# Kernel optimization log

Measured on AMD Instinct MI355X. Metric: run time of the kernel, lower is better.

Reference implementation:

```python
import jax, jax.numpy as jnp
import numpy as np

E = 1024      # d_model
H = 16        # num heads
D = E // H    # head dim = 64
FF = 4096     # dim_feedforward
WIN = 128
EPS = 1e-5    # layer-norm eps
NEG = -1e9


def setup_inputs() -> dict:
    key = jax.random.key(0)
    ks = jax.random.split(key, 16)
    s = 0.02
    f32 = jnp.float32
    return {
        "src":       jax.random.normal(ks[0], (2, 2048, E), f32),
        "in_proj_w": jax.random.normal(ks[1], (3 * E, E), f32) * s,
        "in_proj_b": jnp.zeros((3 * E,), f32),
        "out_w":     jax.random.normal(ks[2], (E, E), f32) * s,
        "out_b":     jnp.zeros((E,), f32),
        "lin1_w":    jax.random.normal(ks[3], (FF, E), f32) * s,
        "lin1_b":    jnp.zeros((FF,), f32),
        "lin2_w":    jax.random.normal(ks[4], (E, FF), f32) * s,
        "lin2_b":    jnp.zeros((E,), f32),
        "ln1_g":     jnp.ones((E,), f32),
        "ln1_beta":  jnp.zeros((E,), f32),
        "ln2_g":     jnp.ones((E,), f32),
        "ln2_beta":  jnp.zeros((E,), f32),
    }


def _layer_norm(x, g, b):
    mu = x.mean(-1, keepdims=True)
    var = ((x - mu) ** 2).mean(-1, keepdims=True)
    return (x - mu) * jax.lax.rsqrt(var + EPS) * g + b


def reference(src, in_proj_w, in_proj_b, out_w, out_b,
              lin1_w, lin1_b, lin2_w, lin2_b,
              ln1_g, ln1_beta, ln2_g, ln2_beta):
    B, L, _ = src.shape  # batch_first=True
    x = src

    # fused QKV projection (torch Linear: y = x @ W.T + b)
    qkv = x @ in_proj_w.T + in_proj_b            # [B, L, 3E]
    q, k, v = jnp.split(qkv, 3, axis=-1)
    q = q.reshape(B, L, H, D)
    k = k.reshape(B, L, H, D)
    v = v.reshape(B, L, H, D)

    scores = jnp.einsum('blhd,bmhd->bhlm', q, k) / np.float32(np.sqrt(D))
    idx = jnp.arange(L)
    band = jnp.abs(idx[:, None] - idx[None, :]) <= WIN   # [L, L] allowed positions
    scores = jnp.where(band, scores, NEG)
    attn = jax.nn.softmax(scores, axis=-1)

    ctx = jnp.einsum('bhlm,bmhd->blhd', attn, v).reshape(B, L, E)
    attn_out = ctx @ out_w.T + out_b

    # post-norm transformer encoder layer (norm_first=False default)
    x = _layer_norm(x + attn_out, ln1_g, ln1_beta)
    ff = jax.nn.relu(x @ lin1_w.T + lin1_b) @ lin2_w.T + lin2_b
    return _layer_norm(x + ff, ln2_g, ln2_beta)
```

## Files before the change

### kernel.cpp

```cpp
#include <hip/hip_runtime.h>
#include <cstdint>
#include <cstddef>


typedef __attribute__((ext_vector_type(8))) short short8;
typedef __attribute__((ext_vector_type(4))) float f32x4;

__device__ __forceinline__ float b2f(unsigned short u) {
  union { unsigned int i; float f; } x; x.i = ((unsigned int)u) << 16; return x.f;
}
__device__ __forceinline__ unsigned short f2b(float f) {
  union { float f; unsigned int i; } x; x.f = f;
  unsigned int i = x.i;
  unsigned int r = (i + 0x7FFFu + ((i >> 16) & 1u)) >> 16;
  return (unsigned short)r;
}
__device__ __forceinline__ uint4 pack8(float4 f0, float4 f1) {
  uint4 r;
  r.x = (unsigned)f2b(f0.x) | ((unsigned)f2b(f0.y) << 16);
  r.y = (unsigned)f2b(f0.z) | ((unsigned)f2b(f0.w) << 16);
  r.z = (unsigned)f2b(f1.x) | ((unsigned)f2b(f1.y) << 16);
  r.w = (unsigned)f2b(f1.z) | ((unsigned)f2b(f1.w) << 16);
  return r;
}

__device__ __forceinline__ void gl_lds16(const unsigned short* g, unsigned short* l) {
  __builtin_amdgcn_global_load_lds(
      (const __attribute__((address_space(1))) unsigned int*)g,
      (__attribute__((address_space(3))) unsigned int*)l, 16, 0, 0);
}

__global__ __launch_bounds__(256) void conv_k(
    const float* __restrict__ in, unsigned short* __restrict__ out, int n)
{
  const int i = (blockIdx.x * 256 + threadIdx.x) * 8;
  if (i < n) {
    const float4 f0 = *(const float4*)(in + i);
    const float4 f1 = *(const float4*)(in + i + 4);
    *(uint4*)(out + i) = pack8(f0, f1);
  }
}

template<int RELU, int OUT32>
__global__ __launch_bounds__(256) void gemm128(
    const unsigned short* __restrict__ A, const unsigned short* __restrict__ Wb,
    const float* __restrict__ bias, void* __restrict__ out,
    int M, int N, int K)
{
  __shared__ unsigned short As[2][128 * 64];
  __shared__ unsigned short Bs[2][128 * 64];

  const int tid = threadIdx.x;
  const int lane = tid & 63, wid = tid >> 6;

  const int nwgx = gridDim.x;
  const int flat = blockIdx.y * nwgx + blockIdx.x;
  const int chunk = (nwgx * gridDim.y) >> 3;
  const int nf = (flat & 7) * chunk + (flat >> 3);
  const int m0 = (nf / nwgx) * 128, n0 = (nf % nwgx) * 128;

  const unsigned short* gA[4];
  const unsigned short* gW[4];
  int ldsO[4];
#pragma unroll
  for (int i = 0; i < 4; ++i) {
    const int sl = wid * 256 + i * 64 + lane;
    const int r = sl >> 3, s = sl & 7, c = (s + r) & 7;
    gA[i] = A + (size_t)(m0 + r) * K + c * 8;
    gW[i] = Wb + (size_t)(n0 + r) * K + c * 8;
    ldsO[i] = (wid * 256 + i * 64) * 8;
  }

  const int cl = lane & 15;
  const int kg = lane >> 4;
  const int msub = (wid >> 1) * 64, nsub = (wid & 1) * 64;
  int aoff[4][2], boff[4][2];
#pragma unroll
  for (int t = 0; t < 4; ++t) {
    const int ar = msub + t * 16 + cl;
    const int br = nsub + t * 16 + cl;
#pragma unroll
    for (int ks = 0; ks < 2; ++ks) {
      aoff[t][ks] = ar * 64 + ((ks * 4 + kg - ar) & 7) * 8;
      boff[t][ks] = br * 64 + ((ks * 4 + kg - br) & 7) * 8;
    }
  }

  f32x4 acc[4][4];
#pragma unroll
  for (int i = 0; i < 4; ++i)
#pragma unroll
    for (int j = 0; j < 4; ++j) acc[i][j] = (f32x4){0.f, 0.f, 0.f, 0.f};

  const int steps = K >> 6;

  const int pre = steps < 2 ? steps : 2;
  for (int t = 0; t < pre; ++t) {
#pragma unroll
    for (int i = 0; i < 4; ++i) { gl_lds16(gA[i], &As[t][ldsO[i]]); gA[i] += 64; }
#pragma unroll
    for (int i = 0; i < 4; ++i) { gl_lds16(gW[i], &Bs[t][ldsO[i]]); gW[i] += 64; }
  }

  int cur = 0;
  for (int s = 0; s < steps; ++s) {
    if (s + 1 < steps) asm volatile("s_waitcnt vmcnt(8)" ::: "memory");
    else               asm volatile("s_waitcnt vmcnt(0)" ::: "memory");
    __builtin_amdgcn_s_barrier();

    short8 af[4][2], bf[4][2];
#pragma unroll
    for (int t = 0; t < 4; ++t) {
      af[t][0] = *(const short8*)&As[cur][aoff[t][0]];
      bf[t][0] = *(const short8*)&Bs[cur][boff[t][0]];
    }
#pragma unroll
    for (int t = 0; t < 4; ++t) {
      af[t][1] = *(const short8*)&As[cur][aoff[t][1]];
      bf[t][1] = *(const short8*)&Bs[cur][boff[t][1]];
    }

    __builtin_amdgcn_s_setprio(1);
#pragma unroll
    for (int mt = 0; mt < 4; ++mt)
#pragma unroll
      for (int nt = 0; nt < 4; ++nt)
        acc[mt][nt] = __builtin_amdgcn_mfma_f32_16x16x32_bf16(af[mt][0], bf[nt][0], acc[mt][nt], 0, 0, 0);
    __builtin_amdgcn_s_setprio(0);

    asm volatile("s_waitcnt lgkmcnt(0)" ::: "memory");
    __builtin_amdgcn_sched_barrier(0);
    __builtin_amdgcn_s_barrier();

    if (s + 2 < steps) {
#pragma unroll
      for (int i = 0; i < 4; ++i) { gl_lds16(gA[i], &As[cur][ldsO[i]]); gA[i] += 64; }
#pragma unroll
      for (int i = 0; i < 4; ++i) { gl_lds16(gW[i], &Bs[cur][ldsO[i]]); gW[i] += 64; }
    }

    __builtin_amdgcn_s_setprio(1);
#pragma unroll
    for (int mt = 0; mt < 4; ++mt)
#pragma unroll
      for (int nt = 0; nt < 4; ++nt)
        acc[mt][nt] = __builtin_amdgcn_mfma_f32_16x16x32_bf16(af[mt][1], bf[nt][1], acc[mt][nt], 0, 0, 0);
    __builtin_amdgcn_s_setprio(0);

    cur ^= 1;
  }

#pragma unroll
  for (int nt = 0; nt < 4; ++nt) {
    const int col = n0 + nsub + nt * 16 + cl;
    const float bvs = bias[col];
#pragma unroll
    for (int mt = 0; mt < 4; ++mt) {
#pragma unroll
      for (int r = 0; r < 4; ++r) {
        const int grow = m0 + msub + mt * 16 + kg * 4 + r;
        float v = acc[mt][nt][r] + bvs;
        if (RELU) v = fmaxf(v, 0.f);
        if (OUT32) ((float*)out)[(size_t)grow * N + col] = v;
        else       ((unsigned short*)out)[(size_t)grow * N + col] = f2b(v);
      }
    }
  }
}

template<int OUT32>
__global__ __launch_bounds__(256) void gemm64(
    const unsigned short* __restrict__ A, const unsigned short* __restrict__ Wb,
    const float* __restrict__ bias, void* __restrict__ out,
    int M, int N, int K)
{
  __shared__ unsigned short As[3][64 * 64];
  __shared__ unsigned short Bs[3][128 * 64];

  const int tid = threadIdx.x;
  const int lane = tid & 63, wid = tid >> 6;

  const int nwgx = gridDim.x;
  const int flat = blockIdx.y * nwgx + blockIdx.x;
  const int chunk = (nwgx * gridDim.y) >> 3;
  const int nf = (flat & 7) * chunk + (flat >> 3);
  const int m0 = (nf / nwgx) * 64, n0 = (nf % nwgx) * 128;

  const unsigned short* gA[2];
  const unsigned short* gW[4];
  int ldsA[2], ldsB[4];
#pragma unroll
  for (int i = 0; i < 2; ++i) {
    const int sl = wid * 128 + i * 64 + lane;
    const int r = sl >> 3, s = sl & 7, c = (s + r) & 7;
    gA[i] = A + (size_t)(m0 + r) * K + c * 8;
    ldsA[i] = (wid * 128 + i * 64) * 8;
  }
#pragma unroll
  for (int i = 0; i < 4; ++i) {
    const int sl = wid * 256 + i * 64 + lane;
    const int r = sl >> 3, s = sl & 7, c = (s + r) & 7;
    gW[i] = Wb + (size_t)(n0 + r) * K + c * 8;
    ldsB[i] = (wid * 256 + i * 64) * 8;
  }

  const int cl = lane & 15;
  const int kg = lane >> 4;
  int aoff[4][2], boff[2][2];
#pragma unroll
  for (int t = 0; t < 4; ++t) {
    const int ar = t * 16 + cl;
#pragma unroll
    for (int ks = 0; ks < 2; ++ks)
      aoff[t][ks] = ar * 64 + ((ks * 4 + kg - ar) & 7) * 8;
  }
#pragma unroll
  for (int t = 0; t < 2; ++t) {
    const int br = wid * 32 + t * 16 + cl;
#pragma unroll
    for (int ks = 0; ks < 2; ++ks)
      boff[t][ks] = br * 64 + ((ks * 4 + kg - br) & 7) * 8;
  }

  f32x4 acc[4][2];
#pragma unroll
  for (int i = 0; i < 4; ++i)
#pragma unroll
    for (int j = 0; j < 2; ++j) acc[i][j] = (f32x4){0.f, 0.f, 0.f, 0.f};

  const int steps = K >> 6;

  const int pre = steps < 3 ? steps : 3;
  for (int t = 0; t < pre; ++t) {
#pragma unroll
    for (int i = 0; i < 2; ++i) { gl_lds16(gA[i], &As[t][ldsA[i]]); gA[i] += 64; }
#pragma unroll
    for (int i = 0; i < 4; ++i) { gl_lds16(gW[i], &Bs[t][ldsB[i]]); gW[i] += 64; }
  }

  int cur = 0;
  for (int s = 0; s < steps; ++s) {
    const int rem = steps - 1 - s;
    if (rem >= 2)      asm volatile("s_waitcnt vmcnt(12)" ::: "memory");
    else if (rem == 1) asm volatile("s_waitcnt vmcnt(6)" ::: "memory");
    else               asm volatile("s_waitcnt vmcnt(0)" ::: "memory");
    __builtin_amdgcn_s_barrier();

    short8 af[4][2], bf[2][2];
#pragma unroll
    for (int t = 0; t < 4; ++t) af[t][0] = *(const short8*)&As[cur][aoff[t][0]];
#pragma unroll
    for (int t = 0; t < 2; ++t) bf[t][0] = *(const short8*)&Bs[cur][boff[t][0]];
#pragma unroll
    for (int t = 0; t < 4; ++t) af[t][1] = *(const short8*)&As[cur][aoff[t][1]];
#pragma unroll
    for (int t = 0; t < 2; ++t) bf[t][1] = *(const short8*)&Bs[cur][boff[t][1]];

    __builtin_amdgcn_s_setprio(1);
#pragma unroll
    for (int mt = 0; mt < 4; ++mt)
#pragma unroll
      for (int nt = 0; nt < 2; ++nt)
        acc[mt][nt] = __builtin_amdgcn_mfma_f32_16x16x32_bf16(af[mt][0], bf[nt][0], acc[mt][nt], 0, 0, 0);
    __builtin_amdgcn_s_setprio(0);

    asm volatile("s_waitcnt lgkmcnt(0)" ::: "memory");
    __builtin_amdgcn_sched_barrier(0);
    __builtin_amdgcn_s_barrier();

    if (s + 3 < steps) {
#pragma unroll
      for (int i = 0; i < 2; ++i) { gl_lds16(gA[i], &As[cur][ldsA[i]]); gA[i] += 64; }
#pragma unroll
      for (int i = 0; i < 4; ++i) { gl_lds16(gW[i], &Bs[cur][ldsB[i]]); gW[i] += 64; }
    }

    __builtin_amdgcn_s_setprio(1);
#pragma unroll
    for (int mt = 0; mt < 4; ++mt)
#pragma unroll
      for (int nt = 0; nt < 2; ++nt)
        acc[mt][nt] = __builtin_amdgcn_mfma_f32_16x16x32_bf16(af[mt][1], bf[nt][1], acc[mt][nt], 0, 0, 0);
    __builtin_amdgcn_s_setprio(0);

    cur = (cur == 2) ? 0 : cur + 1;
  }

#pragma unroll
  for (int nt = 0; nt < 2; ++nt) {
    const int col = n0 + wid * 32 + nt * 16 + cl;
    const float bvs = bias[col];
#pragma unroll
    for (int mt = 0; mt < 4; ++mt) {
#pragma unroll
      for (int r = 0; r < 4; ++r) {
        const int grow = m0 + mt * 16 + kg * 4 + r;
        const float v = acc[mt][nt][r] + bvs;
        if (OUT32) ((float*)out)[(size_t)grow * N + col] = v;
        else       ((unsigned short*)out)[(size_t)grow * N + col] = f2b(v);
      }
    }
  }
}

__global__ __launch_bounds__(256) void attn_mfma(
    const unsigned short* __restrict__ qkv, unsigned short* __restrict__ ctx)
{
  __shared__ unsigned short Ks[64 * 72];
  __shared__ unsigned short Vt[64 * 72];
  __shared__ unsigned short Ps[64 * 72];

  const int tid = threadIdx.x;
  const int bid = blockIdx.x;
  const int qt = bid & 31, h = (bid >> 5) & 15, b = bid >> 9;
  const int q0 = qt * 64;
  const int wstart = max(0, q0 - 128);
  const int wend = min(2048, q0 + 64 + 128);
  const int ntile = (wend - wstart + 63) >> 6;
  const size_t rowb = (size_t)b * 2048;

  const int lane = tid & 63, wid = tid >> 6;
  const int cl = lane & 15;
  const int kq = (lane >> 4) * 8;
  const int rowg = lane >> 4;

  short8 aQ[2];
#pragma unroll
  for (int ks = 0; ks < 2; ++ks)
    aQ[ks] = *(const short8*)(qkv + (rowb + q0 + wid * 16 + cl) * 3072 + h * 64 + ks * 32 + kq);

  float m_i[4], l_i[4];
  f32x4 O[4];
#pragma unroll
  for (int r = 0; r < 4; ++r) { m_i[r] = -1.0e30f; l_i[r] = 0.f; }
#pragma unroll
  for (int nt = 0; nt < 4; ++nt) O[nt] = (f32x4){0.f, 0.f, 0.f, 0.f};

  for (int t = 0; t < ntile; ++t) {
    const int jbase = wstart + t * 64;
    __syncthreads();
    for (int idx = tid; idx < 512; idx += 256) {
      const int r = idx >> 3, c = idx & 7;
      const int jg = jbase + r;
      uint4 kv = {0u, 0u, 0u, 0u}, vv = {0u, 0u, 0u, 0u};
      if (jg < wend) {
        const size_t base = (rowb + jg) * 3072 + h * 64 + c * 8;
        kv = *(const uint4*)(qkv + base + 1024);
        vv = *(const uint4*)(qkv + base + 2048);
      }
      *(uint4*)&Ks[r * 72 + c * 8] = kv;
      const unsigned short* vs = (const unsigned short*)&vv;
#pragma unroll
      for (int ii = 0; ii < 8; ++ii) Vt[(c * 8 + ii) * 72 + r] = vs[ii];
    }
    __syncthreads();

    f32x4 S[4];
#pragma unroll
    for (int nt = 0; nt < 4; ++nt) S[nt] = (f32x4){0.f, 0.f, 0.f, 0.f};
#pragma unroll
    for (int nt = 0; nt < 4; ++nt)
#pragma unroll
      for (int ks = 0; ks < 2; ++ks) {
        const short8 bK = *(const short8*)&Ks[(nt * 16 + cl) * 72 + ks * 32 + kq];
        S[nt] = __builtin_amdgcn_mfma_f32_16x16x32_bf16(aQ[ks], bK, S[nt], 0, 0, 0);
      }

    float sc[4][4];
#pragma unroll
    for (int nt = 0; nt < 4; ++nt) {
      const int jg = jbase + nt * 16 + cl;
#pragma unroll
      for (int r = 0; r < 4; ++r) {
        const int i = q0 + wid * 16 + rowg * 4 + r;
        const bool v = (jg < wend) && (jg >= i - 128) && (jg <= i + 128);
        sc[nt][r] = v ? S[nt][r] * 0.125f : -1.0e30f;
      }
    }

    float alpha[4], p[4][4];
#pragma unroll
    for (int r = 0; r < 4; ++r) {
      float tm = fmaxf(fmaxf(sc[0][r], sc[1][r]), fmaxf(sc[2][r], sc[3][r]));
      tm = fmaxf(tm, __shfl_xor(tm, 1, 64));
      tm = fmaxf(tm, __shfl_xor(tm, 2, 64));
      tm = fmaxf(tm, __shfl_xor(tm, 4, 64));
      tm = fmaxf(tm, __shfl_xor(tm, 8, 64));
      const float mn = fmaxf(m_i[r], tm);
      alpha[r] = __expf(m_i[r] - mn);
      m_i[r] = mn;
      float ps = 0.f;
#pragma unroll
      for (int nt = 0; nt < 4; ++nt) { p[nt][r] = __expf(sc[nt][r] - mn); ps += p[nt][r]; }
      ps += __shfl_xor(ps, 1, 64);
      ps += __shfl_xor(ps, 2, 64);
      ps += __shfl_xor(ps, 4, 64);
      ps += __shfl_xor(ps, 8, 64);
      l_i[r] = l_i[r] * alpha[r] + ps;
    }

#pragma unroll
    for (int nt = 0; nt < 4; ++nt)
#pragma unroll
      for (int r = 0; r < 4; ++r)
        Ps[(wid * 16 + rowg * 4 + r) * 72 + nt * 16 + cl] = f2b(p[nt][r]);
    __syncthreads();

#pragma unroll
    for (int nt = 0; nt < 4; ++nt)
#pragma unroll
      for (int r = 0; r < 4; ++r) O[nt][r] *= alpha[r];
    short8 aP[2];
#pragma unroll
    for (int ks = 0; ks < 2; ++ks)
      aP[ks] = *(const short8*)&Ps[(wid * 16 + cl) * 72 + ks * 32 + kq];
#pragma unroll
    for (int nt = 0; nt < 4; ++nt)
#pragma unroll
      for (int ks = 0; ks < 2; ++ks) {
        const short8 bV = *(const short8*)&Vt[(nt * 16 + cl) * 72 + ks * 32 + kq];
        O[nt] = __builtin_amdgcn_mfma_f32_16x16x32_bf16(aP[ks], bV, O[nt], 0, 0, 0);
      }
  }

#pragma unroll
  for (int nt = 0; nt < 4; ++nt) {
    const int d = nt * 16 + cl;
#pragma unroll
    for (int r = 0; r < 4; ++r) {
      const int i = q0 + wid * 16 + rowg * 4 + r;
      ctx[(rowb + i) * 1024 + h * 64 + d] = f2b(O[nt][r] / l_i[r]);
    }
  }
}

template<int AF32, int BF32, int OF32>
__global__ __launch_bounds__(256) void ln_k(
    const void* __restrict__ a, const void* __restrict__ b,
    const float* __restrict__ g, const float* __restrict__ be,
    void* __restrict__ o)
{
  __shared__ float rbuf[8];
  const int tid = threadIdx.x;
  const size_t base = (size_t)blockIdx.x * 1024;
  const int lane = tid & 63, wid = tid >> 6;

  float xv[4], s = 0.f, sq = 0.f;
#pragma unroll
  for (int t = 0; t < 4; ++t) {
    const int c = tid + t * 256;
    const float av = AF32 ? ((const float*)a)[base + c]
                          : b2f(((const unsigned short*)a)[base + c]);
    const float bv = BF32 ? ((const float*)b)[base + c]
                          : b2f(((const unsigned short*)b)[base + c]);
    const float x = av + bv;
    xv[t] = x; s += x; sq += x * x;
  }
  for (int o2 = 1; o2 < 64; o2 <<= 1) { s += __shfl_xor(s, o2, 64); sq += __shfl_xor(sq, o2, 64); }
  if (lane == 0) { rbuf[wid] = s; rbuf[wid + 4] = sq; }
  __syncthreads();
  s  = rbuf[0] + rbuf[1] + rbuf[2] + rbuf[3];
  sq = rbuf[4] + rbuf[5] + rbuf[6] + rbuf[7];
  const float mean = s * (1.0f / 1024.f);
  const float var = sq * (1.0f / 1024.f) - mean * mean;
  const float rstd = rsqrtf(var + 1e-5f);
#pragma unroll
  for (int t = 0; t < 4; ++t) {
    const int c = tid + t * 256;
    const float y = (xv[t] - mean) * rstd * g[c] + be[c];
    if (OF32) ((float*)o)[base + c] = y;
    else      ((unsigned short*)o)[base + c] = f2b(y);
  }
}

extern "C" void kernel_launch(void* const* d_in, const int* in_sizes, int n_in,
                              void* d_out, int out_size, void* d_ws, size_t ws_size,
                              hipStream_t stream)
{
  (void)in_sizes; (void)n_in; (void)out_size; (void)ws_size;
  const float* src   = (const float*)d_in[0];
  const float* w_in  = (const float*)d_in[1];
  const float* b_in  = (const float*)d_in[2];
  const float* w_out = (const float*)d_in[3];
  const float* b_out = (const float*)d_in[4];
  const float* w1    = (const float*)d_in[5];
  const float* b1    = (const float*)d_in[6];
  const float* w2    = (const float*)d_in[7];
  const float* b2    = (const float*)d_in[8];
  const float* g1    = (const float*)d_in[9];
  const float* be1   = (const float*)d_in[10];
  const float* g2    = (const float*)d_in[11];
  const float* be2   = (const float*)d_in[12];

  char* ws = (char*)d_ws;
  unsigned short* srcb  = (unsigned short*)(ws);
  unsigned short* x1b   = srcb;
  unsigned short* qkv   = (unsigned short*)(ws + 8388608);
  unsigned short* ctx   = (unsigned short*)(ws + 33554432);
  unsigned short* attnb = (unsigned short*)(ws + 8388608);
  unsigned short* ff1   = (unsigned short*)(ws + 8388608);
  unsigned short* wslot = (unsigned short*)(ws + 41943040);
  float*          outf  = (float*)d_out;

  conv_k<<<dim3(2048), 256, 0, stream>>>(src, srcb, 4194304);
  conv_k<<<dim3(1536), 256, 0, stream>>>(w_in, wslot, 3145728);
  gemm128<0, 0><<<dim3(24, 32), 256, 0, stream>>>(srcb, wslot, b_in, qkv, 4096, 3072, 1024);
  attn_mfma<<<dim3(1024), 256, 0, stream>>>(qkv, ctx);
  conv_k<<<dim3(512), 256, 0, stream>>>(w_out, wslot, 1048576);
  gemm64<0><<<dim3(8, 64), 256, 0, stream>>>(ctx, wslot, b_out, attnb, 4096, 1024, 1024);
  ln_k<0, 0, 0><<<dim3(4096), 256, 0, stream>>>(srcb, attnb, g1, be1, x1b);
  conv_k<<<dim3(2048), 256, 0, stream>>>(w1, wslot, 4194304);
  gemm128<1, 0><<<dim3(32, 32), 256, 0, stream>>>(x1b, wslot, b1, ff1, 4096, 4096, 1024);
  conv_k<<<dim3(2048), 256, 0, stream>>>(w2, wslot, 4194304);
  gemm64<1><<<dim3(8, 64), 256, 0, stream>>>(ff1, wslot, b2, outf, 4096, 1024, 4096);
  ln_k<0, 1, 1><<<dim3(4096), 256, 0, stream>>>(x1b, outf, g2, be2, outf);
}
```

Before: 315.3 us.

## Enlarge QKV/FF1 GEMM tiles to 256x256 with 8 waves; reschedule gemm64 MFMAs

Replaces the 128x128, 256-thread GEMM with a 256x256-tile, 512-thread kernel. Each of its 2x4 waves computes a 128x64 sub-tile in two halves, and the fragment loads for the second half are interleaved with the first half's MFMAs. The goal is more data reuse per global byte loaded. In gemm64, all fragments are now loaded before the barrier and all MFMAs issue after the next prefetch, with the setprio hints removed. The trade-off: the large tile needs 128KB of LDS, and the QKV launch drops to 192 workgroups, which underfills the CU count and risks poor occupancy.

```diff
diff --git a/kernel.cpp b/kernel.cpp
--- a/kernel.cpp
+++ b/kernel.cpp
@@ -42,53 +42,43 @@
 }
 
 template<int RELU, int OUT32>
-__global__ __launch_bounds__(256) void gemm128(
+__global__ __launch_bounds__(512, 2) void gemm256(
     const unsigned short* __restrict__ A, const unsigned short* __restrict__ Wb,
     const float* __restrict__ bias, void* __restrict__ out,
     int M, int N, int K)
 {
-  __shared__ unsigned short As[2][128 * 64];
-  __shared__ unsigned short Bs[2][128 * 64];
+  __shared__ unsigned short As[2][256 * 64];
+  __shared__ unsigned short Bs[2][256 * 64];
 
   const int tid = threadIdx.x;
   const int lane = tid & 63, wid = tid >> 6;
-
-  const int nwgx = gridDim.x;
-  const int flat = blockIdx.y * nwgx + blockIdx.x;
-  const int chunk = (nwgx * gridDim.y) >> 3;
+  const int wm = wid >> 2, wn = wid & 3;
+
+  const int gx = gridDim.x;
+  const int flat = blockIdx.y * gx + blockIdx.x;
+  const int chunk = (gx * gridDim.y) >> 3;
   const int nf = (flat & 7) * chunk + (flat >> 3);
-  const int m0 = (nf / nwgx) * 128, n0 = (nf % nwgx) * 128;
+  const int m0 = (nf / gx) * 256, n0 = (nf % gx) * 256;
 
   const unsigned short* gA[4];
   const unsigned short* gW[4];
   int ldsO[4];
 #pragma unroll
   for (int i = 0; i < 4; ++i) {
-    const int sl = wid * 256 + i * 64 + lane;
+    const int sbase = i * 512 + (tid & ~63);
+    const int sl = sbase + lane;
     const int r = sl >> 3, s = sl & 7, c = (s + r) & 7;
     gA[i] = A + (size_t)(m0 + r) * K + c * 8;
     gW[i] = Wb + (size_t)(n0 + r) * K + c * 8;
-    ldsO[i] = (wid * 256 + i * 64) * 8;
+    ldsO[i] = sbase * 8;
   }
 
   const int cl = lane & 15;
   const int kg = lane >> 4;
-  const int msub = (wid >> 1) * 64, nsub = (wid & 1) * 64;
-  int aoff[4][2], boff[4][2];
-#pragma unroll
-  for (int t = 0; t < 4; ++t) {
-    const int ar = msub + t * 16 + cl;
-    const int br = nsub + t * 16 + cl;
-#pragma unroll
-    for (int ks = 0; ks < 2; ++ks) {
-      aoff[t][ks] = ar * 64 + ((ks * 4 + kg - ar) & 7) * 8;
-      boff[t][ks] = br * 64 + ((ks * 4 + kg - br) & 7) * 8;
-    }
-  }
-
-  f32x4 acc[4][4];
-#pragma unroll
-  for (int i = 0; i < 4; ++i)
+
+  f32x4 acc[8][4];
+#pragma unroll
+  for (int i = 0; i < 8; ++i)
 #pragma unroll
     for (int j = 0; j < 4; ++j) acc[i][j] = (f32x4){0.f, 0.f, 0.f, 0.f};
 
@@ -108,25 +98,41 @@
     else               asm volatile("s_waitcnt vmcnt(0)" ::: "memory");
     __builtin_amdgcn_s_barrier();
 
-    short8 af[4][2], bf[4][2];
-#pragma unroll
-    for (int t = 0; t < 4; ++t) {
-      af[t][0] = *(const short8*)&As[cur][aoff[t][0]];
-      bf[t][0] = *(const short8*)&Bs[cur][boff[t][0]];
-    }
-#pragma unroll
-    for (int t = 0; t < 4; ++t) {
-      af[t][1] = *(const short8*)&As[cur][aoff[t][1]];
-      bf[t][1] = *(const short8*)&Bs[cur][boff[t][1]];
-    }
+    short8 bf[4][2];
+#pragma unroll
+    for (int nt = 0; nt < 4; ++nt)
+#pragma unroll
+      for (int ks = 0; ks < 2; ++ks) {
+        const int br = wn * 64 + nt * 16 + cl;
+        bf[nt][ks] = *(const short8*)&Bs[cur][br * 64 + (((ks * 4 + kg) - br) & 7) * 8];
+      }
+    short8 af[4][2];
+#pragma unroll
+    for (int mt = 0; mt < 4; ++mt)
+#pragma unroll
+      for (int ks = 0; ks < 2; ++ks) {
+        const int ar = wm * 128 + mt * 16 + cl;
+        af[mt][ks] = *(const short8*)&As[cur][ar * 64 + (((ks * 4 + kg) - ar) & 7) * 8];
+      }
 
     __builtin_amdgcn_s_setprio(1);
 #pragma unroll
     for (int mt = 0; mt < 4; ++mt)
 #pragma unroll
       for (int nt = 0; nt < 4; ++nt)
-        acc[mt][nt] = __builtin_amdgcn_mfma_f32_16x16x32_bf16(af[mt][0], bf[nt][0], acc[mt][nt], 0, 0, 0);
+#pragma unroll
+        for (int ks = 0; ks < 2; ++ks)
+          acc[mt][nt] = __builtin_amdgcn_mfma_f32_16x16x32_bf16(af[mt][ks], bf[nt][ks], acc[mt][nt], 0, 0, 0);
     __builtin_amdgcn_s_setprio(0);
+
+    short8 ag[4][2];
+#pragma unroll
+    for (int mt = 0; mt < 4; ++mt)
+#pragma unroll
+      for (int ks = 0; ks < 2; ++ks) {
+        const int ar = wm * 128 + (mt + 4) * 16 + cl;
+        ag[mt][ks] = *(const short8*)&As[cur][ar * 64 + (((ks * 4 + kg) - ar) & 7) * 8];
+      }
 
     asm volatile("s_waitcnt lgkmcnt(0)" ::: "memory");
     __builtin_amdgcn_sched_barrier(0);
@@ -144,7 +150,9 @@
     for (int mt = 0; mt < 4; ++mt)
 #pragma unroll
       for (int nt = 0; nt < 4; ++nt)
-        acc[mt][nt] = __builtin_amdgcn_mfma_f32_16x16x32_bf16(af[mt][1], bf[nt][1], acc[mt][nt], 0, 0, 0);
+#pragma unroll
+        for (int ks = 0; ks < 2; ++ks)
+          acc[mt + 4][nt] = __builtin_amdgcn_mfma_f32_16x16x32_bf16(ag[mt][ks], bf[nt][ks], acc[mt + 4][nt], 0, 0, 0);
     __builtin_amdgcn_s_setprio(0);
 
     cur ^= 1;
@@ -152,13 +160,13 @@
 
 #pragma unroll
   for (int nt = 0; nt < 4; ++nt) {
-    const int col = n0 + nsub + nt * 16 + cl;
+    const int col = n0 + wn * 64 + nt * 16 + cl;
     const float bvs = bias[col];
 #pragma unroll
-    for (int mt = 0; mt < 4; ++mt) {
+    for (int mt = 0; mt < 8; ++mt) {
 #pragma unroll
       for (int r = 0; r < 4; ++r) {
-        const int grow = m0 + msub + mt * 16 + kg * 4 + r;
+        const int grow = m0 + wm * 128 + mt * 16 + kg * 4 + r;
         float v = acc[mt][nt][r] + bvs;
         if (RELU) v = fmaxf(v, 0.f);
         if (OUT32) ((float*)out)[(size_t)grow * N + col] = v;
@@ -248,21 +256,13 @@
 
     short8 af[4][2], bf[2][2];
 #pragma unroll
-    for (int t = 0; t < 4; ++t) af[t][0] = *(const short8*)&As[cur][aoff[t][0]];
-#pragma unroll
-    for (int t = 0; t < 2; ++t) bf[t][0] = *(const short8*)&Bs[cur][boff[t][0]];
-#pragma unroll
-    for (int t = 0; t < 4; ++t) af[t][1] = *(const short8*)&As[cur][aoff[t][1]];
-#pragma unroll
-    for (int t = 0; t < 2; ++t) bf[t][1] = *(const short8*)&Bs[cur][boff[t][1]];
-
-    __builtin_amdgcn_s_setprio(1);
-#pragma unroll
-    for (int mt = 0; mt < 4; ++mt)
-#pragma unroll
-      for (int nt = 0; nt < 2; ++nt)
-        acc[mt][nt] = __builtin_amdgcn_mfma_f32_16x16x32_bf16(af[mt][0], bf[nt][0], acc[mt][nt], 0, 0, 0);
-    __builtin_amdgcn_s_setprio(0);
+    for (int t = 0; t < 4; ++t)
+#pragma unroll
+      for (int ks = 0; ks < 2; ++ks) af[t][ks] = *(const short8*)&As[cur][aoff[t][ks]];
+#pragma unroll
+    for (int t = 0; t < 2; ++t)
+#pragma unroll
+      for (int ks = 0; ks < 2; ++ks) bf[t][ks] = *(const short8*)&Bs[cur][boff[t][ks]];
 
     asm volatile("s_waitcnt lgkmcnt(0)" ::: "memory");
     __builtin_amdgcn_sched_barrier(0);
@@ -275,13 +275,13 @@
       for (int i = 0; i < 4; ++i) { gl_lds16(gW[i], &Bs[cur][ldsB[i]]); gW[i] += 64; }
     }
 
-    __builtin_amdgcn_s_setprio(1);
 #pragma unroll
     for (int mt = 0; mt < 4; ++mt)
 #pragma unroll
       for (int nt = 0; nt < 2; ++nt)
-        acc[mt][nt] = __builtin_amdgcn_mfma_f32_16x16x32_bf16(af[mt][1], bf[nt][1], acc[mt][nt], 0, 0, 0);
-    __builtin_amdgcn_s_setprio(0);
+#pragma unroll
+        for (int ks = 0; ks < 2; ++ks)
+          acc[mt][nt] = __builtin_amdgcn_mfma_f32_16x16x32_bf16(af[mt][ks], bf[nt][ks], acc[mt][nt], 0, 0, 0);
 
     cur = (cur == 2) ? 0 : cur + 1;
   }
@@ -504,13 +504,13 @@
 
   conv_k<<<dim3(2048), 256, 0, stream>>>(src, srcb, 4194304);
   conv_k<<<dim3(1536), 256, 0, stream>>>(w_in, wslot, 3145728);
-  gemm128<0, 0><<<dim3(24, 32), 256, 0, stream>>>(srcb, wslot, b_in, qkv, 4096, 3072, 1024);
+  gemm256<0, 0><<<dim3(12, 16), 512, 0, stream>>>(srcb, wslot, b_in, qkv, 4096, 3072, 1024);
   attn_mfma<<<dim3(1024), 256, 0, stream>>>(qkv, ctx);
   conv_k<<<dim3(512), 256, 0, stream>>>(w_out, wslot, 1048576);
   gemm64<0><<<dim3(8, 64), 256, 0, stream>>>(ctx, wslot, b_out, attnb, 4096, 1024, 1024);
   ln_k<0, 0, 0><<<dim3(4096), 256, 0, stream>>>(srcb, attnb, g1, be1, x1b);
   conv_k<<<dim3(2048), 256, 0, stream>>>(w1, wslot, 4194304);
-  gemm128<1, 0><<<dim3(32, 32), 256, 0, stream>>>(x1b, wslot, b1, ff1, 4096, 4096, 1024);
+  gemm256<1, 0><<<dim3(16, 16), 512, 0, stream>>>(x1b, wslot, b1, ff1, 4096, 4096, 1024);
   conv_k<<<dim3(2048), 256, 0, stream>>>(w2, wslot, 4194304);
   gemm64<1><<<dim3(8, 64), 256, 0, stream>>>(ff1, wslot, b2, outf, 4096, 1024, 4096);
   ln_k<0, 1, 1><<<dim3(4096), 256, 0, stream>>>(x1b, outf, g2, be2, outf);
```

Result: no change. 312.0 us (-1.1%).
